# Kernel optimization log

Measured on AMD Instinct MI355X. Metric: run time of the kernel, lower is better.

The kernel has to match this reference:

```python
import jax, jax.numpy as jnp
import numpy as np

B, SEQ, PRED, T = 16, 768, 256, 1024
ENC_IN, MARK, D, H, DH = 7, 4, 512, 8, 64
BUCKET, NH, NB = 32, 4, 32          # NB = T // BUCKET (must be even)
DFF, NLAYERS, COUT = 2048, 2, 7
DEC_LEN = 512
MASK_SELF = -5e4                    # reformer TOKEN_SELF_ATTN_VALUE


def setup_inputs():
    key = jax.random.key(0)
    ks = jax.random.split(key, 16)
    s = 0.02
    return {
        "x_enc": jax.random.normal(ks[0], (B, SEQ, ENC_IN), jnp.float32),
        "x_mark_enc": jax.random.normal(ks[1], (B, SEQ, MARK), jnp.float32),
        "x_dec": jax.random.normal(ks[2], (B, DEC_LEN, ENC_IN), jnp.float32),
        "x_mark_dec": jax.random.normal(ks[3], (B, DEC_LEN, MARK), jnp.float32),
        "conv_w": jax.random.normal(ks[4], (D, ENC_IN, 3), jnp.float32) * s,
        "mark_w": jax.random.normal(ks[5], (MARK, D), jnp.float32) * s,
        "qk_w": jax.random.normal(ks[6], (NLAYERS, D, D), jnp.float32) * s,
        "v_w": jax.random.normal(ks[7], (NLAYERS, D, D), jnp.float32) * s,
        "out_w": jax.random.normal(ks[8], (NLAYERS, D, D), jnp.float32) * s,
        "out_b": jnp.zeros((NLAYERS, D), jnp.float32),
        "ln1_g": jnp.ones((NLAYERS, D), jnp.float32),
        "ln1_b": jnp.zeros((NLAYERS, D), jnp.float32),
        "ln2_g": jnp.ones((NLAYERS, D), jnp.float32),
        "ln2_b": jnp.zeros((NLAYERS, D), jnp.float32),
        "ffn_w1": jax.random.normal(ks[9], (NLAYERS, D, DFF), jnp.float32) * s,
        "ffn_b1": jnp.zeros((NLAYERS, DFF), jnp.float32),
        "ffn_w2": jax.random.normal(ks[10], (NLAYERS, DFF, D), jnp.float32) * s,
        "ffn_b2": jnp.zeros((NLAYERS, D), jnp.float32),
        "lnf_g": jnp.ones((D,), jnp.float32),
        "lnf_b": jnp.zeros((D,), jnp.float32),
        "proj_w": jax.random.normal(ks[11], (D, COUT), jnp.float32) * s,
        "proj_b": jnp.zeros((COUT,), jnp.float32),
        "rotations": jax.random.normal(ks[12], (NLAYERS, DH, NH, NB // 2), jnp.float32),
    }


def _layernorm(x, g, b):
    m = x.mean(-1, keepdims=True)
    v = ((x - m) ** 2).mean(-1, keepdims=True)
    return (x - m) / jnp.sqrt(v + 1e-5) * g + b


def _look_one_back(x):
    # concat each chunk with the previous chunk along the within-chunk axis
    return jnp.concatenate([x, jnp.roll(x, 1, axis=1)], axis=2)


def _lsh_attention(qk, v, rot):
    # shared-QK Reformer LSH attention. qk, v: [bh, t, dh]; rot: [dh, NH, NB//2]
    bh, t, d = qk.shape
    nb = t // BUCKET
    rv = jnp.einsum('btf,fhi->bhti', qk, rot)
    rv = jnp.concatenate([rv, -rv], axis=-1)
    buckets = jnp.argmax(rv, axis=-1) + (jnp.arange(NH) * nb)[None, :, None]
    buckets = buckets.reshape(bh, NH * t)                        # [bh, NH*t]
    ticker = jnp.arange(NH * t) % t
    sticker = jnp.argsort(buckets * t + ticker[None, :], axis=-1)
    undo = jnp.argsort(sticker, axis=-1)
    st = sticker % t                                             # source token ids
    sqk = jnp.take_along_axis(qk, st[..., None], axis=1)         # [bh, NH*t, d]
    sv = jnp.take_along_axis(v, st[..., None], axis=1)
    nc = NH * nb                                                 # number of chunks
    bq = sqk.reshape(bh, nc, BUCKET, d)
    bk = bq / jnp.maximum(jnp.linalg.norm(bq, axis=-1, keepdims=True), 1e-12)
    bv = sv.reshape(bh, nc, BUCKET, d)
    bk, bv = _look_one_back(bk), _look_one_back(bv)
    bq_t = st.reshape(bh, nc, BUCKET)
    bkv_t = _look_one_back(bq_t)
    dots = jnp.einsum('bcie,bcje->bcij', bq, bk) * (d ** -0.5)
    dots = jnp.where(bq_t[..., :, None] == bkv_t[..., None, :], MASK_SELF, dots)
    lse = jax.nn.logsumexp(dots, axis=-1, keepdims=True)
    bo = jnp.einsum('bcij,bcje->bcie', jnp.exp(dots - lse), bv)
    so = bo.reshape(bh, NH * t, d)
    sl = lse.reshape(bh, NH * t)
    o = jnp.take_along_axis(so, undo[..., None], axis=1).reshape(bh, NH, t, d)
    logits = jnp.take_along_axis(sl, undo, axis=1).reshape(bh, NH, t, 1)
    return (o * jax.nn.softmax(logits, axis=1)).sum(axis=1)      # [bh, t, d]


def _lsh_self_attn(x, wqk, wv, wo, bo, rot):
    b, t, _ = x.shape
    qk = (x @ wqk).reshape(b, t, H, DH).transpose(0, 2, 1, 3).reshape(b * H, t, DH)
    v = (x @ wv).reshape(b, t, H, DH).transpose(0, 2, 1, 3).reshape(b * H, t, DH)
    o = _lsh_attention(qk, v, rot)
    o = o.reshape(b, H, t, DH).transpose(0, 2, 1, 3).reshape(b, t, D)
    return o @ wo + bo


def _pos_emb(t, d):
    pos = jnp.arange(t, dtype=jnp.float32)[:, None]
    div = jnp.exp(jnp.arange(0, d, 2, dtype=jnp.float32) * (-np.log(10000.0) / d))
    pe = jnp.zeros((t, d), jnp.float32)
    return pe.at[:, 0::2].set(jnp.sin(pos * div)).at[:, 1::2].set(jnp.cos(pos * div))


def _token_emb(x, w):
    # circular Conv1d(enc_in -> d_model, kernel=3, pad=1, no bias)
    t = x.shape[1]
    xp = jnp.concatenate([x[:, -1:], x, x[:, :1]], axis=1)
    return sum(jnp.einsum('bti,oi->bto', xp[:, k:k + t], w[:, :, k]) for k in range(3))


def _forward(x_enc, x_mark_enc, x_dec, x_mark_dec, conv_w, mark_w, qk_w, v_w,
             out_w, out_b, ln1_g, ln1_b, ln2_g, ln2_b, ffn_w1, ffn_b1,
             ffn_w2, ffn_b2, lnf_g, lnf_b, proj_w, proj_b, rotations):
    x = jnp.concatenate([x_enc, x_dec[:, -PRED:, :]], axis=1)       # [B, T, enc_in]
    xm = jnp.concatenate([x_mark_enc, x_mark_dec[:, -PRED:, :]], axis=1)
    h = _token_emb(x, conv_w) + xm @ mark_w + _pos_emb(T, D)[None]  # [B, T, D]
    for l in range(NLAYERS):
        a = _lsh_self_attn(h, qk_w[l], v_w[l], out_w[l], out_b[l], rotations[l])
        h = _layernorm(h + a, ln1_g[l], ln1_b[l])
        y = jax.nn.gelu(h @ ffn_w1[l] + ffn_b1[l], approximate=False) @ ffn_w2[l] + ffn_b2[l]
        h = _layernorm(h + y, ln2_g[l], ln2_b[l])
    h = _layernorm(h, lnf_g, lnf_b)
    out = h @ proj_w + proj_b
    return out[:, -PRED:, :]


def reference(x_enc, x_mark_enc, x_dec, x_mark_dec, conv_w, mark_w, qk_w, v_w,
              out_w, out_b, ln1_g, ln1_b, ln2_g, ln2_b, ffn_w1, ffn_b1,
              ffn_w2, ffn_b2, lnf_g, lnf_b, proj_w, proj_b, rotations):
    return _forward(x_enc, x_mark_enc, x_dec, x_mark_dec, conv_w, mark_w, qk_w, v_w,
                    out_w, out_b, ln1_g, ln1_b, ln2_g, ln2_b, ffn_w1, ffn_b1,
                    ffn_w2, ffn_b2, lnf_g, lnf_b, proj_w, proj_b, rotations)
```

## Files before the change

### kernel.cpp

```cpp
#include <hip/hip_runtime.h>
#include <math.h>

#define T_ 1024
#define NT_ 4096
#define MASKSELF64 -50000.0
#define MASKSELF32 -50000.0f

typedef short bf16x8 __attribute__((ext_vector_type(8)));
typedef float f32x4 __attribute__((ext_vector_type(4)));

__device__ __forceinline__ unsigned short f2bf(float f) {
  unsigned int x = __float_as_uint(f);
  return (unsigned short)((x + 0x7FFFu + ((x >> 16) & 1u)) >> 16);
}

__global__ __launch_bounds__(256)
void embed_kernel(const float* __restrict__ x_enc, const float* __restrict__ x_mark_enc,
                  const float* __restrict__ x_dec, const float* __restrict__ x_mark_dec,
                  const float* __restrict__ conv_w, const float* __restrict__ mark_w,
                  double* __restrict__ h) {
  int bt = blockIdx.x;
  int b = bt >> 10, t = bt & 1023;
  __shared__ double xs[3][7];
  __shared__ double xm[4];
  int tid = threadIdx.x;
  if (tid < 21) {
    int k = tid / 7, i = tid % 7;
    int tt = t + k - 1;
    if (tt < 0) tt += 1024;
    if (tt >= 1024) tt -= 1024;
    xs[k][i] = (double)((tt < 768) ? x_enc[((size_t)b*768 + tt)*7 + i]
                                   : x_dec[((size_t)b*512 + (tt - 512))*7 + i]);
  }
  if (tid >= 32 && tid < 36) {
    int m = tid - 32;
    xm[m] = (double)((t < 768) ? x_mark_enc[((size_t)b*768 + t)*4 + m]
                               : x_mark_dec[((size_t)b*512 + (t - 512))*4 + m]);
  }
  __syncthreads();
  for (int o = tid; o < 512; o += 256) {
    double acc = 0.0;
    #pragma unroll
    for (int k = 0; k < 3; ++k)
      #pragma unroll
      for (int i = 0; i < 7; ++i)
        acc += xs[k][i] * (double)conv_w[(o*7 + i)*3 + k];
    #pragma unroll
    for (int m = 0; m < 4; ++m) acc += xm[m] * (double)mark_w[m*512 + o];
    int j2 = o & ~1;
    double dv = exp((double)j2 * (-9.210340371976184 / 512.0));
    double arg = (double)t * dv;
    acc += (o & 1) ? cos(arg) : sin(arg);
    h[((size_t)b*1024 + t)*512 + o] = acc;
  }
}

__global__ __launch_bounds__(256)
void dgemm_kernel(const double* __restrict__ A, const float* __restrict__ Bm,
                  const float* __restrict__ bias, double* __restrict__ C,
                  float* __restrict__ C32, int N, int K, int ldb, int flags) {
  __shared__ double As[16][130];
  __shared__ float  Bs[16][132];
  int tid = threadIdx.x;
  int tx = tid & 15, ty = tid >> 4;
  int arow = blockIdx.x * 128;
  int bcol = blockIdx.y * 128;
  int am = tid >> 1, ak = (tid & 1) * 8;
  int bk = tid >> 4, bn = (tid & 15) * 8;
  const double* aptr = A + (size_t)(arow + am)*K + ak;
  const float*  bptr = Bm + (size_t)bk*ldb + bcol + bn;
  double acc[8][8];
  #pragma unroll
  for (int i=0;i<8;++i)
    #pragma unroll
    for (int j=0;j<8;++j) acc[i][j]=0.0;
  double2 av0 = *(const double2*)(aptr + 0);
  double2 av1 = *(const double2*)(aptr + 2);
  double2 av2 = *(const double2*)(aptr + 4);
  double2 av3 = *(const double2*)(aptr + 6);
  float4 bv0 = *(const float4*)(bptr);
  float4 bv1 = *(const float4*)(bptr + 4);
  for (int k0 = 0; k0 < K; k0 += 16) {
    As[ak+0][am] = av0.x; As[ak+1][am] = av0.y;
    As[ak+2][am] = av1.x; As[ak+3][am] = av1.y;
    As[ak+4][am] = av2.x; As[ak+5][am] = av2.y;
    As[ak+6][am] = av3.x; As[ak+7][am] = av3.y;
    *(float4*)&Bs[bk][bn]   = bv0;
    *(float4*)&Bs[bk][bn+4] = bv1;
    __syncthreads();
    if (k0 + 16 < K) {
      aptr += 16;
      bptr += (size_t)16*ldb;
      av0 = *(const double2*)(aptr + 0);
      av1 = *(const double2*)(aptr + 2);
      av2 = *(const double2*)(aptr + 4);
      av3 = *(const double2*)(aptr + 6);
      bv0 = *(const float4*)(bptr);
      bv1 = *(const float4*)(bptr + 4);
    }
    #pragma unroll
    for (int kk=0;kk<16;++kk) {
      double a[8];
      *(double2*)&a[0] = *(const double2*)&As[kk][2*ty];
      *(double2*)&a[2] = *(const double2*)&As[kk][2*ty+32];
      *(double2*)&a[4] = *(const double2*)&As[kk][2*ty+64];
      *(double2*)&a[6] = *(const double2*)&As[kk][2*ty+96];
      float2 f0 = *(const float2*)&Bs[kk][2*tx];
      float2 f1 = *(const float2*)&Bs[kk][2*tx+32];
      float2 f2 = *(const float2*)&Bs[kk][2*tx+64];
      float2 f3 = *(const float2*)&Bs[kk][2*tx+96];
      double b[8];
      b[0]=(double)f0.x; b[1]=(double)f0.y; b[2]=(double)f1.x; b[3]=(double)f1.y;
      b[4]=(double)f2.x; b[5]=(double)f2.y; b[6]=(double)f3.x; b[7]=(double)f3.y;
      #pragma unroll
      for (int i=0;i<8;++i)
        #pragma unroll
        for (int j=0;j<8;++j) acc[i][j] += a[i]*b[j];
    }
    __syncthreads();
  }
  #pragma unroll
  for (int i=0;i<8;++i) {
    int row = arow + 2*ty + (i&1) + 32*(i>>1);
    #pragma unroll
    for (int j=0;j<8;++j) {
      int col = bcol + 2*tx + (j&1) + 32*(j>>1);
      double cv = acc[i][j];
      if (flags & 1) cv += (double)bias[col];
      if (flags & 2) cv = 0.5*cv*(1.0 + erf(cv*0.70710678118654752440));
      if (flags & 4) {
        int b_ = row >> 10, t = row & 1023;
        int hd = col >> 6, dd = col & 63;
        size_t idx = (((size_t)b_*8 + hd)*1024 + t)*64 + dd;
        C[idx] = cv;
        if (flags & 8) C32[idx] = (float)cv;
      } else {
        size_t idx = (size_t)row*N + col;
        if (flags & 16) cv += C[idx];
        C[idx] = cv;
      }
    }
  }
}

__global__ __launch_bounds__(256)
void sgemm_kernel(const float* __restrict__ A, const float* __restrict__ Bm,
                  const float* __restrict__ bias, float* __restrict__ C,
                  int N, int K, int flags) {
  __shared__ float As[16][128];
  __shared__ float Bs[16][128];
  int tid = threadIdx.x;
  int tx = tid & 15, ty = tid >> 4;
  float acc[8][8];
  #pragma unroll
  for (int i=0;i<8;++i)
    #pragma unroll
    for (int j=0;j<8;++j) acc[i][j]=0.f;
  const int arow = blockIdx.x*128;
  const int bcol = blockIdx.y*128;
  int e0 = tid*2, e1 = tid*2 + 1;
  int ra0 = e0 >> 2, ca0 = (e0 & 3)*4;
  int ra1 = e1 >> 2, ca1 = (e1 & 3)*4;
  int kb0 = e0 >> 5, cb0 = (e0 & 31)*4;
  int kb1 = e1 >> 5, cb1 = (e1 & 31)*4;
  const float* pA0 = A + (size_t)(arow + ra0)*K + ca0;
  const float* pA1 = A + (size_t)(arow + ra1)*K + ca1;
  const float* pB0 = Bm + (size_t)kb0*N + bcol + cb0;
  const float* pB1 = Bm + (size_t)kb1*N + bcol + cb1;
  float4 va0 = *(const float4*)pA0;
  float4 va1 = *(const float4*)pA1;
  float4 vb0 = *(const float4*)pB0;
  float4 vb1 = *(const float4*)pB1;
  for (int k0 = 0; k0 < K; k0 += 16) {
    As[ca0+0][ra0]=va0.x; As[ca0+1][ra0]=va0.y; As[ca0+2][ra0]=va0.z; As[ca0+3][ra0]=va0.w;
    As[ca1+0][ra1]=va1.x; As[ca1+1][ra1]=va1.y; As[ca1+2][ra1]=va1.z; As[ca1+3][ra1]=va1.w;
    *(float4*)&Bs[kb0][cb0] = vb0;
    *(float4*)&Bs[kb1][cb1] = vb1;
    __syncthreads();
    if (k0 + 16 < K) {
      pA0 += 16; pA1 += 16;
      pB0 += (size_t)16*N; pB1 += (size_t)16*N;
      va0 = *(const float4*)pA0;
      va1 = *(const float4*)pA1;
      vb0 = *(const float4*)pB0;
      vb1 = *(const float4*)pB1;
    }
    #pragma unroll
    for (int kk=0;kk<16;++kk) {
      float a[8], bb[8];
      #pragma unroll
      for (int i=0;i<8;++i) a[i] = As[kk][ty + 16*i];
      #pragma unroll
      for (int j=0;j<8;++j) bb[j] = Bs[kk][tx + 16*j];
      #pragma unroll
      for (int i=0;i<8;++i)
        #pragma unroll
        for (int j=0;j<8;++j) acc[i][j] += a[i]*bb[j];
    }
    __syncthreads();
  }
  #pragma unroll
  for (int i=0;i<8;++i) {
    int row = arow + ty + 16*i;
    #pragma unroll
    for (int j=0;j<8;++j) {
      int col = bcol + tx + 16*j;
      float cv = acc[i][j];
      if (flags & 1) cv += bias[col];
      if (flags & 2) cv = 0.5f*cv*(1.0f + erff(cv*0.70710678118654752f));
      if (flags & 4) {
        int b = row >> 10, t = row & 1023;
        int hd = col >> 6, dd = col & 63;
        C[(((size_t)b*8 + hd)*1024 + t)*64 + dd] = cv;
      } else {
        C[(size_t)row*N + col] = cv;
      }
    }
  }
}

__global__ __launch_bounds__(256)
void convert_wt_kernel(const float* __restrict__ w, unsigned short* __restrict__ wt,
                       int K, int N) {
  int total = K * N;
  for (int i = blockIdx.x*256 + threadIdx.x; i < total; i += gridDim.x*256) {
    int n = i / K, k = i - n*K;
    wt[i] = f2bf(w[(size_t)k*N + n]);
  }
}

__global__ __launch_bounds__(256)
void bgemm_kernel(const unsigned short* __restrict__ A, const unsigned short* __restrict__ Bt,
                  const float* __restrict__ bias, float* __restrict__ Cf,
                  unsigned short* __restrict__ C16, int N, int K, int flags) {
  __shared__ unsigned short As[128*32];
  __shared__ unsigned short Bs[128*32];
  int tid = threadIdx.x;
  int lane = tid & 63, wave = tid >> 6;
  int wr = wave >> 1, wc = wave & 1;
  int l15 = lane & 15, l4 = lane >> 4;
  int arow = blockIdx.x * 128, bcol = blockIdx.y * 128;
  int s0 = tid, s1 = tid + 256;
  int r0 = s0 >> 2, q0 = s0 & 3;
  int r1 = s1 >> 2, q1 = s1 & 3;
  const unsigned short* pA0 = A + (size_t)(arow + r0)*K + q0*8;
  const unsigned short* pA1 = A + (size_t)(arow + r1)*K + q1*8;
  const unsigned short* pB0 = Bt + (size_t)(bcol + r0)*K + q0*8;
  const unsigned short* pB1 = Bt + (size_t)(bcol + r1)*K + q1*8;
  f32x4 acc[4][4];
  #pragma unroll
  for (int i=0;i<4;++i)
    #pragma unroll
    for (int j=0;j<4;++j)
      #pragma unroll
      for (int r=0;r<4;++r) acc[i][j][r] = 0.f;
  uint4 a0 = *(const uint4*)pA0, a1 = *(const uint4*)pA1;
  uint4 b0 = *(const uint4*)pB0, b1 = *(const uint4*)pB1;
  for (int k0 = 0; k0 < K; k0 += 32) {
    *(uint4*)&As[r0*32 + q0*8] = a0;
    *(uint4*)&As[r1*32 + q1*8] = a1;
    *(uint4*)&Bs[r0*32 + q0*8] = b0;
    *(uint4*)&Bs[r1*32 + q1*8] = b1;
    __syncthreads();
    if (k0 + 32 < K) {
      pA0 += 32; pA1 += 32; pB0 += 32; pB1 += 32;
      a0 = *(const uint4*)pA0; a1 = *(const uint4*)pA1;
      b0 = *(const uint4*)pB0; b1 = *(const uint4*)pB1;
    }
    bf16x8 aF[4], bF[4];
    #pragma unroll
    for (int mt=0; mt<4; ++mt)
      aF[mt] = *(const bf16x8*)&As[(wr*64 + mt*16 + l15)*32 + l4*8];
    #pragma unroll
    for (int nt=0; nt<4; ++nt)
      bF[nt] = *(const bf16x8*)&Bs[(wc*64 + nt*16 + l15)*32 + l4*8];
    #pragma unroll
    for (int mt=0; mt<4; ++mt)
      #pragma unroll
      for (int nt=0; nt<4; ++nt)
        acc[mt][nt] = __builtin_amdgcn_mfma_f32_16x16x32_bf16(aF[mt], bF[nt], acc[mt][nt], 0, 0, 0);
    __syncthreads();
  }
  #pragma unroll
  for (int mt=0; mt<4; ++mt) {
    #pragma unroll
    for (int nt=0; nt<4; ++nt) {
      int col = bcol + wc*64 + nt*16 + l15;
      float bv = (flags & 1) ? bias[col] : 0.f;
      #pragma unroll
      for (int r=0; r<4; ++r) {
        int row = arow + wr*64 + mt*16 + l4*4 + r;
        float cv = acc[mt][nt][r] + bv;
        if (flags & 2) cv = 0.5f*cv*(1.0f + erff(cv*0.70710678118654752f));
        if (flags & 8) C16[(size_t)row*N + col] = f2bf(cv);
        else           Cf[(size_t)row*N + col] = cv;
      }
    }
  }
}

__global__ __launch_bounds__(256)
void bucket_sort_kernel(const double* __restrict__ qk, const float* __restrict__ rot,
                        int* __restrict__ sticker) {
  int bh = blockIdx.x >> 2, r = blockIdx.x & 3;
  __shared__ double rots[64][17];
  __shared__ unsigned char bucket[1024];
  __shared__ int cnt[32];
  __shared__ short H[16][32];
  __shared__ int off2[16][32];
  int tid = threadIdx.x;
  for (int idx = tid; idx < 1024; idx += 256) {
    int f = idx >> 4, i = idx & 15;
    rots[f][i] = (double)rot[(f*4 + r)*16 + i];
  }
  __syncthreads();
  for (int t = tid; t < 1024; t += 256) {
    const double* q = qk + ((size_t)bh*1024 + t)*64;
    double rv[16];
    #pragma unroll
    for (int i=0;i<16;++i) rv[i]=0.0;
    for (int f=0; f<64; ++f) {
      double qf = q[f];
      #pragma unroll
      for (int i=0;i<16;++i) rv[i] += qf * rots[f][i];
    }
    int best = 0; double bv = rv[0];
    #pragma unroll
    for (int i=1;i<16;++i) if (rv[i] > bv) { bv=rv[i]; best=i; }
    #pragma unroll
    for (int i=0;i<16;++i) { double nv = -rv[i]; if (nv > bv) { bv=nv; best=16+i; } }
    bucket[t] = (unsigned char)best;
  }
  __syncthreads();
  {
    int c = tid >> 4, s = tid & 15;
    int h0 = 0, h1 = 0;
    for (int t = c*64; t < c*64 + 64; ++t) {
      int b = bucket[t];
      h0 += (b == s);
      h1 += (b == s + 16);
    }
    H[c][s] = (short)h0;
    H[c][s+16] = (short)h1;
  }
  __syncthreads();
  if (tid < 32) {
    int s = 0;
    for (int c = 0; c < 16; ++c) s += H[c][tid];
    cnt[tid] = s;
  }
  __syncthreads();
  if (tid < 32) {
    int o = 0;
    for (int b = 0; b < tid; ++b) o += cnt[b];
    for (int c = 0; c < 16; ++c) { off2[c][tid] = o; o += H[c][tid]; }
  }
  __syncthreads();
  int* outp = sticker + (size_t)bh*NT_ + r*1024;
  #pragma unroll
  for (int q = 0; q < 2; ++q) {
    int p = tid + q*256;
    int c = p >> 5, b = p & 31;
    int pos = off2[c][b];
    for (int t = c*64; t < c*64 + 64; ++t)
      if (bucket[t] == (unsigned char)b) outp[pos++] = t;
  }
}

__global__ __launch_bounds__(256)
void lsh_attn_kernel(const double* __restrict__ qk, const double* __restrict__ v,
                     const int* __restrict__ sticker,
                     double* __restrict__ obuf, double* __restrict__ lse, int bh0) {
  int bh_l = blockIdx.x >> 7;
  int bh = bh0 + bh_l;
  int c  = blockIdx.x & 127;
  int cprev = (c + 127) & 127;
  __shared__ double kv[64][66];
  __shared__ double pp[32][66];
  __shared__ double rnorm[64];
  __shared__ int tk[64];
  int tid = threadIdx.x;
  if (tid < 64) {
    int chunk = (tid < 32) ? c : cprev;
    tk[tid] = sticker[(size_t)bh*NT_ + chunk*32 + (tid & 31)];
  }
  __syncthreads();
  for (int idx = tid; idx < 2048; idx += 256) {
    int j = idx >> 5, c2 = (idx & 31)*2;
    *(double2*)&kv[j][c2] = *(const double2*)(qk + ((size_t)bh*1024 + tk[j])*64 + c2);
  }
  __syncthreads();
  if (tid < 64) {
    double s = 0.0;
    #pragma unroll
    for (int f=0; f<64; ++f) { double x = kv[tid][f]; s += x*x; }
    rnorm[tid] = 1.0 / fmax(sqrt(s), 1e-12);
  }
  __syncthreads();
  int i = tid >> 3, sub = tid & 7;
  int ti = tk[i];
  double dots[8];
  double dmax = -1.0e300;
  #pragma unroll
  for (int jj=0; jj<8; ++jj) {
    int j = sub*8 + jj;
    double s = 0.0;
    #pragma unroll
    for (int f=0; f<64; ++f) s += kv[i][f] * kv[j][f];
    s *= rnorm[j] * 0.125;
    if (ti == tk[j]) s = MASKSELF64;
    dots[jj] = s;
    dmax = fmax(dmax, s);
  }
  #pragma unroll
  for (int w=1; w<8; w<<=1) dmax = fmax(dmax, __shfl_xor(dmax, w, 64));
  double esum = 0.0;
  #pragma unroll
  for (int jj=0; jj<8; ++jj) {
    double e = exp(dots[jj] - dmax);
    esum += e;
    pp[i][sub*8+jj] = e;
  }
  #pragma unroll
  for (int w=1; w<8; w<<=1) esum += __shfl_xor(esum, w, 64);
  __syncthreads();
  for (int idx = tid; idx < 2048; idx += 256) {
    int j = idx >> 5, c2 = (idx & 31)*2;
    *(double2*)&kv[j][c2] = *(const double2*)(v + ((size_t)bh*1024 + tk[j])*64 + c2);
  }
  __syncthreads();
  double ov[8];
  #pragma unroll
  for (int dd=0;dd<8;++dd) ov[dd]=0.0;
  for (int j=0;j<64;++j) {
    double p = pp[i][j];
    #pragma unroll
    for (int dd=0;dd<8;++dd) ov[dd] += p * kv[j][sub*8+dd];
  }
  double rinv = 1.0 / esum;
  int r = c >> 5;
  size_t ob = (((size_t)bh_l*4 + r)*1024 + ti)*64 + sub*8;
  #pragma unroll
  for (int dd=0;dd<8;++dd) obuf[ob + dd] = ov[dd]*rinv;
  if (sub == 0) lse[((size_t)bh*4 + r)*1024 + ti] = log(esum) + dmax;
}

__global__ __launch_bounds__(256)
void combine_kernel(const double* __restrict__ obuf, const double* __restrict__ lse,
                    double* __restrict__ comb, int bh0) {
  int g = blockIdx.x*4 + (threadIdx.x >> 6);
  int bh_l = g >> 10, t = g & 1023;
  int bh = bh0 + bh_l;
  int d = threadIdx.x & 63;
  double l[4];
  #pragma unroll
  for (int r=0;r<4;++r) l[r] = lse[((size_t)bh*4 + r)*1024 + t];
  double m = fmax(fmax(l[0],l[1]), fmax(l[2],l[3]));
  double e[4], s=0.0;
  #pragma unroll
  for (int r=0;r<4;++r){ e[r]=exp(l[r]-m); s+=e[r]; }
  double rs = 1.0/s;
  double o = 0.0;
  #pragma unroll
  for (int r=0;r<4;++r)
    o += e[r]*rs * obuf[(((size_t)bh_l*4 + r)*1024 + t)*64 + d];
  int b = bh >> 3, hd = bh & 7;
  comb[((size_t)b*1024 + t)*512 + hd*64 + d] = o;
}

__global__ __launch_bounds__(256)
void lsh_attn32_kernel(const float* __restrict__ qk, const float* __restrict__ v,
                       const int* __restrict__ sticker,
                       float* __restrict__ obuf, float* __restrict__ lse, int bh0) {
  int bh_l = blockIdx.x >> 7;
  int bh = bh0 + bh_l;
  int c  = blockIdx.x & 127;
  int cprev = (c + 127) & 127;
  __shared__ float kv[64][68];
  __shared__ float pp[32][68];
  __shared__ float rnorm[64];
  __shared__ int tk[64];
  int tid = threadIdx.x;
  if (tid < 64) {
    int chunk = (tid < 32) ? c : cprev;
    tk[tid] = sticker[(size_t)bh*NT_ + chunk*32 + (tid & 31)];
  }
  __syncthreads();
  for (int idx = tid; idx < 1024; idx += 256) {
    int j = idx >> 4, c4 = (idx & 15)*4;
    *(float4*)&kv[j][c4] = *(const float4*)(qk + ((size_t)bh*1024 + tk[j])*64 + c4);
  }
  __syncthreads();
  if (tid < 64) {
    float s = 0.f;
    #pragma unroll
    for (int f=0; f<64; ++f) { float x = kv[tid][f]; s += x*x; }
    rnorm[tid] = 1.0f / fmaxf(sqrtf(s), 1e-12f);
  }
  __syncthreads();
  int i = tid >> 3, sub = tid & 7;
  int ti = tk[i];
  float dots[8];
  float dmax = -1.0e30f;
  #pragma unroll
  for (int jj=0; jj<8; ++jj) {
    int j = sub*8 + jj;
    float s = 0.f;
    #pragma unroll
    for (int f=0; f<64; ++f) s += kv[i][f] * kv[j][f];
    s *= rnorm[j] * 0.125f;
    if (ti == tk[j]) s = MASKSELF32;
    dots[jj] = s;
    dmax = fmaxf(dmax, s);
  }
  #pragma unroll
  for (int w=1; w<8; w<<=1) dmax = fmaxf(dmax, __shfl_xor(dmax, w, 64));
  float esum = 0.f;
  #pragma unroll
  for (int jj=0; jj<8; ++jj) {
    float e = expf(dots[jj] - dmax);
    esum += e;
    pp[i][sub*8+jj] = e;
  }
  #pragma unroll
  for (int w=1; w<8; w<<=1) esum += __shfl_xor(esum, w, 64);
  __syncthreads();
  for (int idx = tid; idx < 1024; idx += 256) {
    int j = idx >> 4, c4 = (idx & 15)*4;
    *(float4*)&kv[j][c4] = *(const float4*)(v + ((size_t)bh*1024 + tk[j])*64 + c4);
  }
  __syncthreads();
  float ov[8];
  #pragma unroll
  for (int dd=0;dd<8;++dd) ov[dd]=0.f;
  for (int j=0;j<64;++j) {
    float p = pp[i][j];
    #pragma unroll
    for (int dd=0;dd<8;++dd) ov[dd] += p * kv[j][sub*8+dd];
  }
  float rinv = 1.0f / esum;
  int r = c >> 5;
  size_t ob = (((size_t)bh_l*4 + r)*1024 + ti)*64 + sub*8;
  #pragma unroll
  for (int dd=0;dd<8;++dd) obuf[ob + dd] = ov[dd]*rinv;
  if (sub == 0) lse[((size_t)bh*4 + r)*1024 + ti] = logf(esum) + dmax;
}

__global__ __launch_bounds__(256)
void combine32_kernel(const float* __restrict__ obuf, const float* __restrict__ lse,
                      float* __restrict__ comb, int bh0) {
  int g = blockIdx.x*4 + (threadIdx.x >> 6);
  int bh_l = g >> 10, t = g & 1023;
  int bh = bh0 + bh_l;
  int d = threadIdx.x & 63;
  float l[4];
  #pragma unroll
  for (int r=0;r<4;++r) l[r] = lse[((size_t)bh*4 + r)*1024 + t];
  float m = fmaxf(fmaxf(l[0],l[1]), fmaxf(l[2],l[3]));
  float e[4], s=0.f;
  #pragma unroll
  for (int r=0;r<4;++r){ e[r]=expf(l[r]-m); s+=e[r]; }
  float rs = 1.0f/s;
  float o = 0.f;
  #pragma unroll
  for (int r=0;r<4;++r)
    o += e[r]*rs * obuf[(((size_t)bh_l*4 + r)*1024 + t)*64 + d];
  int b = bh >> 3, hd = bh & 7;
  comb[((size_t)b*1024 + t)*512 + hd*64 + d] = o;
}

__global__ __launch_bounds__(256)
void ln_kernel(const double* __restrict__ x, const double* __restrict__ res,
               const float* __restrict__ gw, const float* __restrict__ bw,
               double* __restrict__ outp, float* __restrict__ out32) {
  int row = blockIdx.x;
  int tid = threadIdx.x;
  const double* xr = x + (size_t)row*512;
  double v0 = xr[tid], v1 = xr[tid+256];
  if (res) { const double* rr = res + (size_t)row*512; v0 += rr[tid]; v1 += rr[tid+256]; }
  double s = v0 + v1;
  #pragma unroll
  for (int w=1; w<64; w<<=1) s += __shfl_xor(s, w, 64);
  __shared__ double red[4];
  int wid = tid >> 6, lane = tid & 63;
  if (lane == 0) red[wid] = s;
  __syncthreads();
  s = red[0]+red[1]+red[2]+red[3];
  double m = s * (1.0/512.0);
  double d0 = v0 - m, d1 = v1 - m;
  double q = d0*d0 + d1*d1;
  #pragma unroll
  for (int w=1; w<64; w<<=1) q += __shfl_xor(q, w, 64);
  __syncthreads();
  if (lane == 0) red[wid] = q;
  __syncthreads();
  q = red[0]+red[1]+red[2]+red[3];
  double var = q * (1.0/512.0);
  double rstd = 1.0 / sqrt(var + 1e-5);
  double o0 = d0*rstd*(double)gw[tid] + (double)bw[tid];
  double o1 = d1*rstd*(double)gw[tid+256] + (double)bw[tid+256];
  outp[(size_t)row*512 + tid]       = o0;
  outp[(size_t)row*512 + tid + 256] = o1;
  if (out32) {
    out32[(size_t)row*512 + tid]       = (float)o0;
    out32[(size_t)row*512 + tid + 256] = (float)o1;
  }
}

__global__ __launch_bounds__(256)
void lnmx_kernel(const double* __restrict__ x, const float* __restrict__ res,
                 const float* __restrict__ gw, const float* __restrict__ bw,
                 float* __restrict__ out32, unsigned short* __restrict__ out16) {
  int row = blockIdx.x;
  int tid = threadIdx.x;
  const double* xr = x + (size_t)row*512;
  const float*  rr = res + (size_t)row*512;
  double v0 = xr[tid] + (double)rr[tid];
  double v1 = xr[tid+256] + (double)rr[tid+256];
  double s = v0 + v1;
  #pragma unroll
  for (int w=1; w<64; w<<=1) s += __shfl_xor(s, w, 64);
  __shared__ double red[4];
  int wid = tid >> 6, lane = tid & 63;
  if (lane == 0) red[wid] = s;
  __syncthreads();
  s = red[0]+red[1]+red[2]+red[3];
  double m = s * (1.0/512.0);
  double d0 = v0 - m, d1 = v1 - m;
  double q = d0*d0 + d1*d1;
  #pragma unroll
  for (int w=1; w<64; w<<=1) q += __shfl_xor(q, w, 64);
  __syncthreads();
  if (lane == 0) red[wid] = q;
  __syncthreads();
  q = red[0]+red[1]+red[2]+red[3];
  double rstd = 1.0 / sqrt(q * (1.0/512.0) + 1e-5);
  float o0 = (float)(d0*rstd*(double)gw[tid] + (double)bw[tid]);
  float o1 = (float)(d1*rstd*(double)gw[tid+256] + (double)bw[tid+256]);
  out32[(size_t)row*512 + tid]       = o0;
  out32[(size_t)row*512 + tid + 256] = o1;
  out16[(size_t)row*512 + tid]       = f2bf(o0);
  out16[(size_t)row*512 + tid + 256] = f2bf(o1);
}

__global__ __launch_bounds__(256)
void ln32_kernel(const float* __restrict__ x, const float* __restrict__ res,
                 const float* __restrict__ gw, const float* __restrict__ bw,
                 float* __restrict__ out32) {
  int row = blockIdx.x;
  int tid = threadIdx.x;
  const float* xr = x + (size_t)row*512;
  double v0 = (double)xr[tid], v1 = (double)xr[tid+256];
  if (res) { const float* rr = res + (size_t)row*512; v0 += (double)rr[tid]; v1 += (double)rr[tid+256]; }
  double s = v0 + v1;
  #pragma unroll
  for (int w=1; w<64; w<<=1) s += __shfl_xor(s, w, 64);
  __shared__ double red[4];
  int wid = tid >> 6, lane = tid & 63;
  if (lane == 0) red[wid] = s;
  __syncthreads();
  s = red[0]+red[1]+red[2]+red[3];
  double m = s * (1.0/512.0);
  double d0 = v0 - m, d1 = v1 - m;
  double q = d0*d0 + d1*d1;
  #pragma unroll
  for (int w=1; w<64; w<<=1) q += __shfl_xor(q, w, 64);
  __syncthreads();
  if (lane == 0) red[wid] = q;
  __syncthreads();
  q = red[0]+red[1]+red[2]+red[3];
  double rstd = 1.0 / sqrt(q * (1.0/512.0) + 1e-5);
  out32[(size_t)row*512 + tid]       = (float)(d0*rstd*(double)gw[tid] + (double)bw[tid]);
  out32[(size_t)row*512 + tid + 256] = (float)(d1*rstd*(double)gw[tid+256] + (double)bw[tid+256]);
}

__global__ __launch_bounds__(64)
void proj_kernel(const float* __restrict__ hf, const float* __restrict__ pw,
                 const float* __restrict__ pb, float* __restrict__ outp) {
  int row = blockIdx.x;
  int b = row >> 8, tp = row & 255;
  const float* hr = hf + ((size_t)b*1024 + 768 + tp)*512;
  int lane = threadIdx.x;
  double acc[7];
  #pragma unroll
  for (int cc=0;cc<7;++cc) acc[cc]=0.0;
  for (int d = lane; d < 512; d += 64) {
    double hv = (double)hr[d];
    #pragma unroll
    for (int cc=0;cc<7;++cc) acc[cc] += hv * (double)pw[d*7 + cc];
  }
  #pragma unroll
  for (int cc=0;cc<7;++cc) {
    double s = acc[cc];
    #pragma unroll
    for (int w=32;w>=1;w>>=1) s += __shfl_xor(s, w, 64);
    if (lane == 0) outp[(size_t)row*7 + cc] = (float)(s + (double)pb[cc]);
  }
}

extern "C" void kernel_launch(void* const* d_in, const int* in_sizes, int n_in,
                              void* d_out, int out_size, void* d_ws, size_t ws_size,
                              hipStream_t stream) {
  (void)in_sizes; (void)n_in; (void)out_size; (void)ws_size;
  const float* x_enc      = (const float*)d_in[0];
  const float* x_mark_enc = (const float*)d_in[1];
  const float* x_dec      = (const float*)d_in[2];
  const float* x_mark_dec = (const float*)d_in[3];
  const float* conv_w     = (const float*)d_in[4];
  const float* mark_w     = (const float*)d_in[5];
  const float* qk_w       = (const float*)d_in[6];
  const float* v_w        = (const float*)d_in[7];
  const float* out_w      = (const float*)d_in[8];
  const float* out_b      = (const float*)d_in[9];
  const float* ln1_g      = (const float*)d_in[10];
  const float* ln1_b      = (const float*)d_in[11];
  const float* ln2_g      = (const float*)d_in[12];
  const float* ln2_b      = (const float*)d_in[13];
  const float* ffn_w1     = (const float*)d_in[14];
  const float* ffn_b1     = (const float*)d_in[15];
  const float* ffn_w2     = (const float*)d_in[16];
  const float* ffn_b2     = (const float*)d_in[17];
  const float* lnf_g      = (const float*)d_in[18];
  const float* lnf_b      = (const float*)d_in[19];
  const float* proj_w     = (const float*)d_in[20];
  const float* proj_b     = (const float*)d_in[21];
  const float* rotations  = (const float*)d_in[22];

  char* ws = (char*)d_ws;
  double* h64   = (double*)(ws);
  double* qk64  = (double*)(ws + 67108864);
  double* v64   = (double*)(ws + 134217728);
  double* obuf  = (double*)(ws + 201326592);
  int*    stick = (int*)   (ws + 234881024);
  double* lse64 = (double*)(ws + 236978176);
  float*  lse32 = (float*) (ws + 236978176);
  unsigned short* w1t = (unsigned short*)(ws + 241172480);
  unsigned short* w2t = (unsigned short*)(ws + 243269632);
  double* comb  = v64;
  float* h32    = (float*)(ws + 201326592);
  float* qk32   = (float*)(ws + 134217728);
  float* v32    = (float*)(ws + 167772160);
  float* obuf32 = (float*)(ws + 67108864);
  float* comb32 = (float*)(ws + 100663296);
  float* ao32   = (float*)(ws + 201326592);
  float* hA32   = (float*)(ws + 134217728);
  unsigned short* hA16  = (unsigned short*)(ws + 67108864);
  unsigned short* hid16 = (unsigned short*)(ws);
  float* y32    = (float*)(ws + 167772160);
  float* h2f    = (float*)(ws + 201326592);
  float* hf32   = (float*)(ws + 67108864);

  embed_kernel<<<16384, 256, 0, stream>>>(x_enc, x_mark_enc, x_dec, x_mark_dec,
                                          conv_w, mark_w, h64);
  convert_wt_kernel<<<2048, 256, 0, stream>>>(ffn_w1 + 1048576, w1t, 512, 2048);
  convert_wt_kernel<<<2048, 256, 0, stream>>>(ffn_w2 + 1048576, w2t, 2048, 512);

  dgemm_kernel<<<dim3(128,4), 256, 0, stream>>>(h64, qk_w, nullptr, qk64, nullptr,
                                                512, 512, 512, 4);
  dgemm_kernel<<<dim3(128,4), 256, 0, stream>>>(h64, v_w, nullptr, v64, nullptr,
                                                512, 512, 512, 4);
  bucket_sort_kernel<<<512, 256, 0, stream>>>(qk64, rotations, stick);
  for (int g = 0; g < 8; ++g) {
    lsh_attn_kernel<<<2048, 256, 0, stream>>>(qk64, v64, stick, obuf, lse64, g*16);
    combine_kernel<<<4096, 256, 0, stream>>>(obuf, lse64, comb, g*16);
  }
  dgemm_kernel<<<dim3(128,4), 256, 0, stream>>>(comb, out_w, out_b, qk64, nullptr,
                                                512, 512, 512, 1);
  ln_kernel<<<16384, 256, 0, stream>>>(h64, qk64, ln1_g, ln1_b, h64, nullptr);
  for (int c = 0; c < 4; ++c) {
    dgemm_kernel<<<dim3(128,4), 256, 0, stream>>>(h64, ffn_w1 + c*512,
                                                  ffn_b1 + c*512, qk64, nullptr,
                                                  512, 512, 2048, 3);
    dgemm_kernel<<<dim3(128,4), 256, 0, stream>>>(qk64, ffn_w2 + (size_t)c*512*512,
                                                  ffn_b2, comb, nullptr,
                                                  512, 512, 512, (c == 0) ? 1 : 16);
  }
  ln_kernel<<<16384, 256, 0, stream>>>(h64, comb, ln2_g, ln2_b, h64, h32);

  sgemm_kernel<<<dim3(128,4), 256, 0, stream>>>(h32, v_w + 262144, nullptr, v32,
                                                512, 512, 4);
  dgemm_kernel<<<dim3(128,4), 256, 0, stream>>>(h64, qk_w + 262144, nullptr, qk64, qk32,
                                                512, 512, 512, 4 | 8);
  bucket_sort_kernel<<<512, 256, 0, stream>>>(qk64, rotations + 4096, stick);
  for (int g = 0; g < 4; ++g) {
    lsh_attn32_kernel<<<4096, 256, 0, stream>>>(qk32, v32, stick, obuf32, lse32, g*32);
    combine32_kernel<<<8192, 256, 0, stream>>>(obuf32, lse32, comb32, g*32);
  }
  sgemm_kernel<<<dim3(128,4), 256, 0, stream>>>(comb32, out_w + 262144, out_b + 512,
                                                ao32, 512, 512, 1);
  lnmx_kernel<<<16384, 256, 0, stream>>>(h64, ao32, ln1_g + 512, ln1_b + 512, hA32, hA16);
  bgemm_kernel<<<dim3(128,16), 256, 0, stream>>>(hA16, w1t, ffn_b1 + 2048,
                                                 nullptr, hid16, 2048, 512, 1|2|8);
  bgemm_kernel<<<dim3(128,4), 256, 0, stream>>>(hid16, w2t, ffn_b2 + 512,
                                                y32, nullptr, 512, 2048, 1);
  ln32_kernel<<<16384, 256, 0, stream>>>(hA32, y32, ln2_g + 512, ln2_b + 512, h2f);
  ln32_kernel<<<16384, 256, 0, stream>>>(h2f, nullptr, lnf_g, lnf_b, hf32);
  proj_kernel<<<4096, 64, 0, stream>>>(hf32, proj_w, proj_b, (float*)d_out);
}
```

Before: 4.608 ms.

## Move layer-2 V and output projections to bf16 MFMA, shrink dgemm tile

Replaces the fp32 SIMT sgemm for the second layer's V projection and attention output projection with the bf16 MFMA bgemm. To feed it, the layer norm and combine kernels now emit bf16 and the weights are pre-transposed to bf16. The dgemm tile drops from 128 to 64 rows so twice as many blocks launch, and the bgemm shared tiles are padded to 40 columns to reduce LDS bank conflicts. The cost is lower precision in the layer-2 V and output path, which could move results closer to the tolerance.

Measured after the change: 4.552 ms (median of 2 runs). About the same (-1.2%).

```diff
diff --git a/kernel.cpp b/kernel.cpp
--- a/kernel.cpp
+++ b/kernel.cpp
@@ -59,32 +59,28 @@
 void dgemm_kernel(const double* __restrict__ A, const float* __restrict__ Bm,
                   const float* __restrict__ bias, double* __restrict__ C,
                   float* __restrict__ C32, int N, int K, int ldb, int flags) {
-  __shared__ double As[16][130];
+  __shared__ double As[16][66];
   __shared__ float  Bs[16][132];
   int tid = threadIdx.x;
   int tx = tid & 15, ty = tid >> 4;
-  int arow = blockIdx.x * 128;
+  int arow = blockIdx.x * 64;
   int bcol = blockIdx.y * 128;
-  int am = tid >> 1, ak = (tid & 1) * 8;
+  int am = tid >> 2, ak = (tid & 3) * 4;
   int bk = tid >> 4, bn = (tid & 15) * 8;
   const double* aptr = A + (size_t)(arow + am)*K + ak;
   const float*  bptr = Bm + (size_t)bk*ldb + bcol + bn;
-  double acc[8][8];
-  #pragma unroll
-  for (int i=0;i<8;++i)
+  double acc[4][8];
+  #pragma unroll
+  for (int i=0;i<4;++i)
     #pragma unroll
     for (int j=0;j<8;++j) acc[i][j]=0.0;
   double2 av0 = *(const double2*)(aptr + 0);
   double2 av1 = *(const double2*)(aptr + 2);
-  double2 av2 = *(const double2*)(aptr + 4);
-  double2 av3 = *(const double2*)(aptr + 6);
   float4 bv0 = *(const float4*)(bptr);
   float4 bv1 = *(const float4*)(bptr + 4);
   for (int k0 = 0; k0 < K; k0 += 16) {
     As[ak+0][am] = av0.x; As[ak+1][am] = av0.y;
     As[ak+2][am] = av1.x; As[ak+3][am] = av1.y;
-    As[ak+4][am] = av2.x; As[ak+5][am] = av2.y;
-    As[ak+6][am] = av3.x; As[ak+7][am] = av3.y;
     *(float4*)&Bs[bk][bn]   = bv0;
     *(float4*)&Bs[bk][bn+4] = bv1;
     __syncthreads();
@@ -93,38 +89,29 @@
       bptr += (size_t)16*ldb;
       av0 = *(const double2*)(aptr + 0);
       av1 = *(const double2*)(aptr + 2);
-      av2 = *(const double2*)(aptr + 4);
-      av3 = *(const double2*)(aptr + 6);
       bv0 = *(const float4*)(bptr);
       bv1 = *(const float4*)(bptr + 4);
     }
     #pragma unroll
     for (int kk=0;kk<16;++kk) {
-      double a[8];
-      *(double2*)&a[0] = *(const double2*)&As[kk][2*ty];
-      *(double2*)&a[2] = *(const double2*)&As[kk][2*ty+32];
-      *(double2*)&a[4] = *(const double2*)&As[kk][2*ty+64];
-      *(double2*)&a[6] = *(const double2*)&As[kk][2*ty+96];
-      float2 f0 = *(const float2*)&Bs[kk][2*tx];
-      float2 f1 = *(const float2*)&Bs[kk][2*tx+32];
-      float2 f2 = *(const float2*)&Bs[kk][2*tx+64];
-      float2 f3 = *(const float2*)&Bs[kk][2*tx+96];
-      double b[8];
-      b[0]=(double)f0.x; b[1]=(double)f0.y; b[2]=(double)f1.x; b[3]=(double)f1.y;
-      b[4]=(double)f2.x; b[5]=(double)f2.y; b[6]=(double)f3.x; b[7]=(double)f3.y;
+      double a[4], b[8];
       #pragma unroll
-      for (int i=0;i<8;++i)
+      for (int i=0;i<4;++i) a[i] = As[kk][ty + 16*i];
+      #pragma unroll
+      for (int j=0;j<8;++j) b[j] = (double)Bs[kk][tx + 16*j];
+      #pragma unroll
+      for (int i=0;i<4;++i)
         #pragma unroll
         for (int j=0;j<8;++j) acc[i][j] += a[i]*b[j];
     }
     __syncthreads();
   }
   #pragma unroll
-  for (int i=0;i<8;++i) {
-    int row = arow + 2*ty + (i&1) + 32*(i>>1);
+  for (int i=0;i<4;++i) {
+    int row = arow + ty + 16*i;
     #pragma unroll
     for (int j=0;j<8;++j) {
-      int col = bcol + 2*tx + (j&1) + 32*(j>>1);
+      int col = bcol + tx + 16*j;
       double cv = acc[i][j];
       if (flags & 1) cv += (double)bias[col];
       if (flags & 2) cv = 0.5*cv*(1.0 + erf(cv*0.70710678118654752440));
@@ -144,82 +131,6 @@
 }
 
 __global__ __launch_bounds__(256)
-void sgemm_kernel(const float* __restrict__ A, const float* __restrict__ Bm,
-                  const float* __restrict__ bias, float* __restrict__ C,
-                  int N, int K, int flags) {
-  __shared__ float As[16][128];
-  __shared__ float Bs[16][128];
-  int tid = threadIdx.x;
-  int tx = tid & 15, ty = tid >> 4;
-  float acc[8][8];
-  #pragma unroll
-  for (int i=0;i<8;++i)
-    #pragma unroll
-    for (int j=0;j<8;++j) acc[i][j]=0.f;
-  const int arow = blockIdx.x*128;
-  const int bcol = blockIdx.y*128;
-  int e0 = tid*2, e1 = tid*2 + 1;
-  int ra0 = e0 >> 2, ca0 = (e0 & 3)*4;
-  int ra1 = e1 >> 2, ca1 = (e1 & 3)*4;
-  int kb0 = e0 >> 5, cb0 = (e0 & 31)*4;
-  int kb1 = e1 >> 5, cb1 = (e1 & 31)*4;
-  const float* pA0 = A + (size_t)(arow + ra0)*K + ca0;
-  const float* pA1 = A + (size_t)(arow + ra1)*K + ca1;
-  const float* pB0 = Bm + (size_t)kb0*N + bcol + cb0;
-  const float* pB1 = Bm + (size_t)kb1*N + bcol + cb1;
-  float4 va0 = *(const float4*)pA0;
-  float4 va1 = *(const float4*)pA1;
-  float4 vb0 = *(const float4*)pB0;
-  float4 vb1 = *(const float4*)pB1;
-  for (int k0 = 0; k0 < K; k0 += 16) {
-    As[ca0+0][ra0]=va0.x; As[ca0+1][ra0]=va0.y; As[ca0+2][ra0]=va0.z; As[ca0+3][ra0]=va0.w;
-    As[ca1+0][ra1]=va1.x; As[ca1+1][ra1]=va1.y; As[ca1+2][ra1]=va1.z; As[ca1+3][ra1]=va1.w;
-    *(float4*)&Bs[kb0][cb0] = vb0;
-    *(float4*)&Bs[kb1][cb1] = vb1;
-    __syncthreads();
-    if (k0 + 16 < K) {
-      pA0 += 16; pA1 += 16;
-      pB0 += (size_t)16*N; pB1 += (size_t)16*N;
-      va0 = *(const float4*)pA0;
-      va1 = *(const float4*)pA1;
-      vb0 = *(const float4*)pB0;
-      vb1 = *(const float4*)pB1;
-    }
-    #pragma unroll
-    for (int kk=0;kk<16;++kk) {
-      float a[8], bb[8];
-      #pragma unroll
-      for (int i=0;i<8;++i) a[i] = As[kk][ty + 16*i];
-      #pragma unroll
-      for (int j=0;j<8;++j) bb[j] = Bs[kk][tx + 16*j];
-      #pragma unroll
-      for (int i=0;i<8;++i)
-        #pragma unroll
-        for (int j=0;j<8;++j) acc[i][j] += a[i]*bb[j];
-    }
-    __syncthreads();
-  }
-  #pragma unroll
-  for (int i=0;i<8;++i) {
-    int row = arow + ty + 16*i;
-    #pragma unroll
-    for (int j=0;j<8;++j) {
-      int col = bcol + tx + 16*j;
-      float cv = acc[i][j];
-      if (flags & 1) cv += bias[col];
-      if (flags & 2) cv = 0.5f*cv*(1.0f + erff(cv*0.70710678118654752f));
-      if (flags & 4) {
-        int b = row >> 10, t = row & 1023;
-        int hd = col >> 6, dd = col & 63;
-        C[(((size_t)b*8 + hd)*1024 + t)*64 + dd] = cv;
-      } else {
-        C[(size_t)row*N + col] = cv;
-      }
-    }
-  }
-}
-
-__global__ __launch_bounds__(256)
 void convert_wt_kernel(const float* __restrict__ w, unsigned short* __restrict__ wt,
                        int K, int N) {
   int total = K * N;
@@ -233,8 +144,8 @@
 void bgemm_kernel(const unsigned short* __restrict__ A, const unsigned short* __restrict__ Bt,
                   const float* __restrict__ bias, float* __restrict__ Cf,
                   unsigned short* __restrict__ C16, int N, int K, int flags) {
-  __shared__ unsigned short As[128*32];
-  __shared__ unsigned short Bs[128*32];
+  __shared__ unsigned short As[128*40];
+  __shared__ unsigned short Bs[128*40];
   int tid = threadIdx.x;
   int lane = tid & 63, wave = tid >> 6;
   int wr = wave >> 1, wc = wave & 1;
@@ -257,10 +168,10 @@
   uint4 a0 = *(const uint4*)pA0, a1 = *(const uint4*)pA1;
   uint4 b0 = *(const uint4*)pB0, b1 = *(const uint4*)pB1;
   for (int k0 = 0; k0 < K; k0 += 32) {
-    *(uint4*)&As[r0*32 + q0*8] = a0;
-    *(uint4*)&As[r1*32 + q1*8] = a1;
-    *(uint4*)&Bs[r0*32 + q0*8] = b0;
-    *(uint4*)&Bs[r1*32 + q1*8] = b1;
+    *(uint4*)&As[r0*40 + q0*8] = a0;
+    *(uint4*)&As[r1*40 + q1*8] = a1;
+    *(uint4*)&Bs[r0*40 + q0*8] = b0;
+    *(uint4*)&Bs[r1*40 + q1*8] = b1;
     __syncthreads();
     if (k0 + 32 < K) {
       pA0 += 32; pA1 += 32; pB0 += 32; pB1 += 32;
@@ -270,10 +181,10 @@
     bf16x8 aF[4], bF[4];
     #pragma unroll
     for (int mt=0; mt<4; ++mt)
-      aF[mt] = *(const bf16x8*)&As[(wr*64 + mt*16 + l15)*32 + l4*8];
+      aF[mt] = *(const bf16x8*)&As[(wr*64 + mt*16 + l15)*40 + l4*8];
     #pragma unroll
     for (int nt=0; nt<4; ++nt)
-      bF[nt] = *(const bf16x8*)&Bs[(wc*64 + nt*16 + l15)*32 + l4*8];
+      bF[nt] = *(const bf16x8*)&Bs[(wc*64 + nt*16 + l15)*40 + l4*8];
     #pragma unroll
     for (int mt=0; mt<4; ++mt)
       #pragma unroll
@@ -292,8 +203,15 @@
         int row = arow + wr*64 + mt*16 + l4*4 + r;
         float cv = acc[mt][nt][r] + bv;
         if (flags & 2) cv = 0.5f*cv*(1.0f + erff(cv*0.70710678118654752f));
-        if (flags & 8) C16[(size_t)row*N + col] = f2bf(cv);
-        else           Cf[(size_t)row*N + col] = cv;
+        if (flags & 4) {
+          int b_ = row >> 10, t = row & 1023;
+          int hd = col >> 6, dd = col & 63;
+          Cf[(((size_t)b_*8 + hd)*1024 + t)*64 + dd] = cv;
+        } else if (flags & 8) {
+          C16[(size_t)row*N + col] = f2bf(cv);
+        } else {
+          Cf[(size_t)row*N + col] = cv;
+        }
       }
     }
   }
@@ -548,7 +466,7 @@
 
 __global__ __launch_bounds__(256)
 void combine32_kernel(const float* __restrict__ obuf, const float* __restrict__ lse,
-                      float* __restrict__ comb, int bh0) {
+                      unsigned short* __restrict__ comb16, int bh0) {
   int g = blockIdx.x*4 + (threadIdx.x >> 6);
   int bh_l = g >> 10, t = g & 1023;
   int bh = bh0 + bh_l;
@@ -566,13 +484,14 @@
   for (int r=0;r<4;++r)
     o += e[r]*rs * obuf[(((size_t)bh_l*4 + r)*1024 + t)*64 + d];
   int b = bh >> 3, hd = bh & 7;
-  comb[((size_t)b*1024 + t)*512 + hd*64 + d] = o;
+  comb16[((size_t)b*1024 + t)*512 + hd*64 + d] = f2bf(o);
 }
 
 __global__ __launch_bounds__(256)
 void ln_kernel(const double* __restrict__ x, const double* __restrict__ res,
                const float* __restrict__ gw, const float* __restrict__ bw,
-               double* __restrict__ outp, float* __restrict__ out32) {
+               double* __restrict__ outp, float* __restrict__ out32,
+               unsigned short* __restrict__ out16) {
   int row = blockIdx.x;
   int tid = threadIdx.x;
   const double* xr = x + (size_t)row*512;
@@ -604,6 +523,10 @@
   if (out32) {
     out32[(size_t)row*512 + tid]       = (float)o0;
     out32[(size_t)row*512 + tid + 256] = (float)o1;
+  }
+  if (out16) {
+    out16[(size_t)row*512 + tid]       = f2bf((float)o0);
+    out16[(size_t)row*512 + tid + 256] = f2bf((float)o1);
   }
 }
 
@@ -736,12 +659,14 @@
   float*  lse32 = (float*) (ws + 236978176);
   unsigned short* w1t = (unsigned short*)(ws + 241172480);
   unsigned short* w2t = (unsigned short*)(ws + 243269632);
+  unsigned short* vwt = (unsigned short*)(ws + 245366784);
+  unsigned short* owt = (unsigned short*)(ws + 245891072);
   double* comb  = v64;
-  float* h32    = (float*)(ws + 201326592);
+  unsigned short* h16 = (unsigned short*)(ws + 67108864);
   float* qk32   = (float*)(ws + 134217728);
   float* v32    = (float*)(ws + 167772160);
   float* obuf32 = (float*)(ws + 67108864);
-  float* comb32 = (float*)(ws + 100663296);
+  unsigned short* comb16 = (unsigned short*)(ws + 100663296);
   float* ao32   = (float*)(ws + 201326592);
   float* hA32   = (float*)(ws + 134217728);
   unsigned short* hA16  = (unsigned short*)(ws + 67108864);
@@ -754,40 +679,42 @@
                                           conv_w, mark_w, h64);
   convert_wt_kernel<<<2048, 256, 0, stream>>>(ffn_w1 + 1048576, w1t, 512, 2048);
   convert_wt_kernel<<<2048, 256, 0, stream>>>(ffn_w2 + 1048576, w2t, 2048, 512);
-
-  dgemm_kernel<<<dim3(128,4), 256, 0, stream>>>(h64, qk_w, nullptr, qk64, nullptr,
+  convert_wt_kernel<<<512, 256, 0, stream>>>(v_w + 262144, vwt, 512, 512);
+  convert_wt_kernel<<<512, 256, 0, stream>>>(out_w + 262144, owt, 512, 512);
+
+  dgemm_kernel<<<dim3(256,4), 256, 0, stream>>>(h64, qk_w, nullptr, qk64, nullptr,
                                                 512, 512, 512, 4);
-  dgemm_kernel<<<dim3(128,4), 256, 0, stream>>>(h64, v_w, nullptr, v64, nullptr,
+  dgemm_kernel<<<dim3(256,4), 256, 0, stream>>>(h64, v_w, nullptr, v64, nullptr,
                                                 512, 512, 512, 4);
   bucket_sort_kernel<<<512, 256, 0, stream>>>(qk64, rotations, stick);
   for (int g = 0; g < 8; ++g) {
     lsh_attn_kernel<<<2048, 256, 0, stream>>>(qk64, v64, stick, obuf, lse64, g*16);
     combine_kernel<<<4096, 256, 0, stream>>>(obuf, lse64, comb, g*16);
   }
-  dgemm_kernel<<<dim3(128,4), 256, 0, stream>>>(comb, out_w, out_b, qk64, nullptr,
+  dgemm_kernel<<<dim3(256,4), 256, 0, stream>>>(comb, out_w, out_b, qk64, nullptr,
                                                 512, 512, 512, 1);
-  ln_kernel<<<16384, 256, 0, stream>>>(h64, qk64, ln1_g, ln1_b, h64, nullptr);
+  ln_kernel<<<16384, 256, 0, stream>>>(h64, qk64, ln1_g, ln1_b, h64, nullptr, nullptr);
   for (int c = 0; c < 4; ++c) {
-    dgemm_kernel<<<dim3(128,4), 256, 0, stream>>>(h64, ffn_w1 + c*512,
+    dgemm_kernel<<<dim3(256,4), 256, 0, stream>>>(h64, ffn_w1 + c*512,
                                                   ffn_b1 + c*512, qk64, nullptr,
                                                   512, 512, 2048, 3);
-    dgemm_kernel<<<dim3(128,4), 256, 0, stream>>>(qk64, ffn_w2 + (size_t)c*512*512,
+    dgemm_kernel<<<dim3(256,4), 256, 0, stream>>>(qk64, ffn_w2 + (size_t)c*512*512,
                                                   ffn_b2, comb, nullptr,
                                                   512, 512, 512, (c == 0) ? 1 : 16);
   }
-  ln_kernel<<<16384, 256, 0, stream>>>(h64, comb, ln2_g, ln2_b, h64, h32);
-
-  sgemm_kernel<<<dim3(128,4), 256, 0, stream>>>(h32, v_w + 262144, nullptr, v32,
+  ln_kernel<<<16384, 256, 0, stream>>>(h64, comb, ln2_g, ln2_b, h64, nullptr, h16);
+
+  bgemm_kernel<<<dim3(128,4), 256, 0, stream>>>(h16, vwt, nullptr, v32, nullptr,
                                                 512, 512, 4);
-  dgemm_kernel<<<dim3(128,4), 256, 0, stream>>>(h64, qk_w + 262144, nullptr, qk64, qk32,
+  dgemm_kernel<<<dim3(256,4), 256, 0, stream>>>(h64, qk_w + 262144, nullptr, qk64, qk32,
                                                 512, 512, 512, 4 | 8);
   bucket_sort_kernel<<<512, 256, 0, stream>>>(qk64, rotations + 4096, stick);
   for (int g = 0; g < 4; ++g) {
     lsh_attn32_kernel<<<4096, 256, 0, stream>>>(qk32, v32, stick, obuf32, lse32, g*32);
-    combine32_kernel<<<8192, 256, 0, stream>>>(obuf32, lse32, comb32, g*32);
-  }
-  sgemm_kernel<<<dim3(128,4), 256, 0, stream>>>(comb32, out_w + 262144, out_b + 512,
-                                                ao32, 512, 512, 1);
+    combine32_kernel<<<8192, 256, 0, stream>>>(obuf32, lse32, comb16, g*32);
+  }
+  bgemm_kernel<<<dim3(128,4), 256, 0, stream>>>(comb16, owt, out_b + 512, ao32, nullptr,
+                                                512, 512, 1);
   lnmx_kernel<<<16384, 256, 0, stream>>>(h64, ao32, ln1_g + 512, ln1_b + 512, hA32, hA16);
   bgemm_kernel<<<dim3(128,16), 256, 0, stream>>>(hA16, w1t, ffn_b1 + 2048,
                                                  nullptr, hid16, 2048, 512, 1|2|8);
```
